# Performance work log

Hardware: AMD Instinct MI355X
Metric: run time of the kernel (lower is better)

Reference implementation:

```python
import jax, jax.numpy as jnp
import numpy as np

N_NODES = 100000


def gcn_conv(x, W, b, src, dst, n):
    """PyG GCNConv: add self-loops, symmetric degree norm, linear, scatter-add."""
    loop = jnp.arange(n, dtype=src.dtype)
    s = jnp.concatenate([src, loop])  # source nodes (message origin)
    d = jnp.concatenate([dst, loop])  # target nodes (aggregation)
    deg = jax.ops.segment_sum(jnp.ones_like(d, dtype=x.dtype), d, num_segments=n)
    dinv = jnp.where(deg > 0, jax.lax.rsqrt(deg), 0.0)
    norm = dinv[s] * dinv[d]  # [E+N]
    h = x @ W  # [N, out]
    msg = h[s] * norm[:, None]  # [E+N, out]
    return jax.ops.segment_sum(msg, d, num_segments=n) + b


def setup_inputs() -> dict:
    key = jax.random.key(0)
    ks = jax.random.split(key, 8)
    n, e, din, dh, dout = N_NODES, 3200000, 128, 64, 6
    x = jax.random.normal(ks[0], (n, din), dtype=jnp.float32)
    edge_index = jax.random.randint(ks[1], (2, e), 0, n, dtype=jnp.int64)
    sc = lambda f: 1.0 / np.sqrt(f)
    W1 = jax.random.normal(ks[2], (din, dh), dtype=jnp.float32) * sc(din)
    b1 = jnp.zeros((dh,), dtype=jnp.float32)
    W2 = jax.random.normal(ks[3], (dh, dh), dtype=jnp.float32) * sc(dh)
    b2 = jnp.zeros((dh,), dtype=jnp.float32)
    W3 = jax.random.normal(ks[4], (dh, dout), dtype=jnp.float32) * sc(dh)
    b3 = jnp.zeros((dout,), dtype=jnp.float32)
    return {"x": x, "edge_index": edge_index, "W1": W1, "b1": b1,
            "W2": W2, "b2": b2, "W3": W3, "b3": b3}


def reference(x, edge_index, W1, b1, W2, b2, W3, b3):
    n = x.shape[0]
    src, dst = edge_index[0], edge_index[1]
    # eval mode: dropout is identity
    h = jax.nn.relu(gcn_conv(x, W1, b1, src, dst, n))
    h = jax.nn.relu(gcn_conv(h, W2, b2, src, dst, n))
    h = gcn_conv(h, W3, b3, src, dst, n)
    return jax.nn.log_softmax(h, axis=1)
```

## Files before the change

### kernel.cpp

```cpp
#include <hip/hip_runtime.h>
#include <hip/hip_fp16.h>
#include <math.h>


#define WS_ALIGN(x) (((x) + 255) & ~(size_t)255)
#define BKN 128
#define CAP 4608
#define EPT 8
#define BIN_THR 512
#define BIN_CHUNK (BIN_THR * EPT)

typedef _Float16 half8 __attribute__((ext_vector_type(8)));
typedef float floatx4 __attribute__((ext_vector_type(4)));

__global__ __launch_bounds__(BIN_THR) void bin_kernel(
    const int* __restrict__ src, const int* __restrict__ dst,
    int* __restrict__ cur, int* __restrict__ slab, int E, int NB) {
    __shared__ int counts[784];
    const int tid = threadIdx.x;
    const int base = blockIdx.x * BIN_CHUNK + tid * EPT;
    for (int i = tid; i < NB; i += BIN_THR) counts[i] = 0;
    __syncthreads();
    int b[EPT], w[EPT], lpos[EPT];
    #pragma unroll
    for (int k = 0; k < EPT; ++k) {
        int e = base + k;
        if (e < E) {
            int s = src[e], d = dst[e];
            b[k] = d >> 7;
            w[k] = (s << 7) | (d & 127);
        } else b[k] = -1;
    }
    #pragma unroll
    for (int k = 0; k < EPT; ++k)
        if (b[k] >= 0) lpos[k] = atomicAdd(&counts[b[k]], 1);
    __syncthreads();
    for (int i = tid; i < NB; i += BIN_THR) {
        int c = counts[i];
        counts[i] = c ? atomicAdd(&cur[i], c) : 0;
    }
    __syncthreads();
    #pragma unroll
    for (int k = 0; k < EPT; ++k) {
        if (b[k] >= 0) {
            int pos = counts[b[k]] + lpos[k];
            if (pos < CAP) slab[(size_t)b[k] * CAP + pos] = w[k];
        }
    }
}

__global__ __launch_bounds__(512) void bucket_sort_kernel(
    const int* __restrict__ slab, const int* __restrict__ cur,
    int* __restrict__ srcS, int2* __restrict__ rows,
    float* __restrict__ dinv, int n) {
    __shared__ int cnt[BKN], s[BKN], cursor[BKN];
    const int b = blockIdx.x, tid = threadIdx.x;
    const int m = min(cur[b], CAP);
    const int* sp = slab + (size_t)b * CAP;
    if (tid < BKN) cnt[tid] = 0;
    __syncthreads();
    for (int j = tid; j < m; j += 512) atomicAdd(&cnt[sp[j] & (BKN - 1)], 1);
    __syncthreads();
    if (tid < BKN) s[tid] = cnt[tid];
    __syncthreads();
    for (int off = 1; off < BKN; off <<= 1) {
        int v = 0;
        if (tid < BKN && tid >= off) v = s[tid - off];
        __syncthreads();
        if (tid < BKN) s[tid] += v;
        __syncthreads();
    }
    if (tid < BKN) {
        int ofs = s[tid] - cnt[tid];
        cursor[tid] = ofs;
        int node = b * BKN + tid;
        if (node < n) {
            rows[node] = make_int2(b * CAP + ofs, b * CAP + ofs + cnt[tid]);
            dinv[node] = rsqrtf((float)(cnt[tid] + 1));
        }
    }
    __syncthreads();
    for (int j = tid; j < m; j += 512) {
        int w = sp[j];
        int p = atomicAdd(&cursor[w & (BKN - 1)], 1);
        srcS[(size_t)b * CAP + p] = w >> 7;
    }
}

template <int K>
__global__ __launch_bounds__(256) void linear_mfma_f32_kernel(
    const float* __restrict__ Xf, const float* __restrict__ W,
    const float* __restrict__ dinv, _Float16* __restrict__ Y, int n) {
    constexpr int KC = K / 32;
    __shared__ _Float16 Bf[KC * 4 * 64 * 8];
    const int tid = threadIdx.x;
    for (int i = tid; i < KC * 4 * 64 * 8; i += 256) {
        int j = i & 7, lane = (i >> 3) & 63, tile = (i >> 9) & 3, kc = i >> 11;
        int k = kc * 32 + ((lane >> 4) << 3) + j;
        int col = tile * 16 + (lane & 15);
        Bf[i] = (_Float16)W[k * 64 + col];
    }
    __syncthreads();
    const int lane = tid & 63, wid = tid >> 6;
    const int mrow = lane & 15, quad = lane >> 4;
    #pragma unroll
    for (int tt = 0; tt < 4; ++tt) {
        const int base = (blockIdx.x * 4 + tt) * 64 + wid * 16;
        if (base >= n) continue;
        const int anode = min(base + mrow, n - 1);
        floatx4 acc[4] = {{0, 0, 0, 0}, {0, 0, 0, 0}, {0, 0, 0, 0}, {0, 0, 0, 0}};
        #pragma unroll
        for (int kc = 0; kc < KC; ++kc) {
            float4 xa = *(const float4*)&Xf[(size_t)anode * K + kc * 32 + quad * 8];
            float4 xb = *(const float4*)&Xf[(size_t)anode * K + kc * 32 + quad * 8 + 4];
            half8 a;
            a[0] = (_Float16)xa.x; a[1] = (_Float16)xa.y; a[2] = (_Float16)xa.z; a[3] = (_Float16)xa.w;
            a[4] = (_Float16)xb.x; a[5] = (_Float16)xb.y; a[6] = (_Float16)xb.z; a[7] = (_Float16)xb.w;
            #pragma unroll
            for (int t = 0; t < 4; ++t) {
                half8 b = *(const half8*)&Bf[((kc * 4 + t) * 64 + lane) * 8];
                acc[t] = __builtin_amdgcn_mfma_f32_16x16x32_f16(a, b, acc[t], 0, 0, 0);
            }
        }
        #pragma unroll
        for (int r = 0; r < 4; ++r) {
            int node = base + quad * 4 + r;
            if (node < n) {
                float di = dinv[node];
                #pragma unroll
                for (int t = 0; t < 4; ++t)
                    Y[(size_t)node * 64 + t * 16 + mrow] = (_Float16)(acc[t][r] * di);
            }
        }
    }
}

__global__ __launch_bounds__(256) void linear_mfma_f16_kernel(
    const _Float16* __restrict__ Xh, const float* __restrict__ W,
    const float* __restrict__ dinv, _Float16* __restrict__ Y, int n) {
    constexpr int K = 64, KC = 2;
    __shared__ _Float16 Bf[KC * 4 * 64 * 8];
    const int tid = threadIdx.x;
    for (int i = tid; i < KC * 4 * 64 * 8; i += 256) {
        int j = i & 7, lane = (i >> 3) & 63, tile = (i >> 9) & 3, kc = i >> 11;
        int k = kc * 32 + ((lane >> 4) << 3) + j;
        int col = tile * 16 + (lane & 15);
        Bf[i] = (_Float16)W[k * 64 + col];
    }
    __syncthreads();
    const int lane = tid & 63, wid = tid >> 6;
    const int mrow = lane & 15, quad = lane >> 4;
    #pragma unroll
    for (int tt = 0; tt < 4; ++tt) {
        const int base = (blockIdx.x * 4 + tt) * 64 + wid * 16;
        if (base >= n) continue;
        const int anode = min(base + mrow, n - 1);
        floatx4 acc[4] = {{0, 0, 0, 0}, {0, 0, 0, 0}, {0, 0, 0, 0}, {0, 0, 0, 0}};
        #pragma unroll
        for (int kc = 0; kc < KC; ++kc) {
            half8 a = *(const half8*)&Xh[(size_t)anode * K + kc * 32 + quad * 8];
            #pragma unroll
            for (int t = 0; t < 4; ++t) {
                half8 b = *(const half8*)&Bf[((kc * 4 + t) * 64 + lane) * 8];
                acc[t] = __builtin_amdgcn_mfma_f32_16x16x32_f16(a, b, acc[t], 0, 0, 0);
            }
        }
        #pragma unroll
        for (int r = 0; r < 4; ++r) {
            int node = base + quad * 4 + r;
            if (node < n) {
                float di = dinv[node];
                #pragma unroll
                for (int t = 0; t < 4; ++t)
                    Y[(size_t)node * 64 + t * 16 + mrow] = (_Float16)(acc[t][r] * di);
            }
        }
    }
}

__global__ __launch_bounds__(256) void linear3_kernel(const __half* __restrict__ Xh,
                                                      const float* __restrict__ W,
                                                      const float* __restrict__ dinv,
                                                      __half* __restrict__ Y, int n) {
    __shared__ float Wl[64 * 6];
    __shared__ float Xs[32][65];
    const int tid = threadIdx.x;
    for (int i = tid; i < 64 * 6; i += 256) Wl[i] = W[i];
    const int sub = tid >> 3;
    const int feat = tid & 7;
    for (int base = blockIdx.x * 32; base < n; base += gridDim.x * 32) {
        __syncthreads();
        for (int i = tid; i < 32 * 64; i += 256) {
            int r = i >> 6, c = i & 63;
            int node = base + r;
            Xs[r][c] = (node < n) ? __half2float(Xh[(size_t)node * 64 + c]) : 0.f;
        }
        __syncthreads();
        int node = base + sub;
        if (node < n) {
            float r = 0.f;
            if (feat < 6) {
                float acc = 0.f;
                #pragma unroll
                for (int k = 0; k < 64; ++k) acc = fmaf(Xs[sub][k], Wl[k * 6 + feat], acc);
                r = acc * dinv[node];
            }
            Y[(size_t)node * 8 + feat] = __float2half_rn(r);
        }
    }
}

__global__ __launch_bounds__(256) void agg64_kernel(
    const _Float16* __restrict__ Hs, const float* __restrict__ dinv,
    const int* __restrict__ srcS, const int2* __restrict__ rows,
    const float* __restrict__ bias, _Float16* __restrict__ Out,
    int n, int do_relu) {
    const int wave = (blockIdx.x * blockDim.x + threadIdx.x) >> 6;
    const int lane = threadIdx.x & 63;
    if (wave >= n) return;
    const int slot = lane >> 3;
    const int f8 = lane & 7;
    const int2 row = rows[wave];
    const int beg = row.x, end = row.y;
    half8 hA, hB;
    #pragma unroll
    for (int i = 0; i < 8; ++i) { hA[i] = (_Float16)0.f; hB[i] = (_Float16)0.f; }
    int j = beg;
    for (; j + 32 <= end; j += 32) {
        int s0 = srcS[j      + slot];
        int s1 = srcS[j + 8  + slot];
        int s2 = srcS[j + 16 + slot];
        int s3 = srcS[j + 24 + slot];
        half8 v0 = *(const half8*)&Hs[(size_t)s0 * 64 + f8 * 8];
        half8 v1 = *(const half8*)&Hs[(size_t)s1 * 64 + f8 * 8];
        half8 v2 = *(const half8*)&Hs[(size_t)s2 * 64 + f8 * 8];
        half8 v3 = *(const half8*)&Hs[(size_t)s3 * 64 + f8 * 8];
        hA += v0; hB += v1; hA += v2; hB += v3;
    }
    for (; j + 16 <= end; j += 16) {
        int s0 = srcS[j + slot];
        int s1 = srcS[j + 8 + slot];
        half8 v0 = *(const half8*)&Hs[(size_t)s0 * 64 + f8 * 8];
        half8 v1 = *(const half8*)&Hs[(size_t)s1 * 64 + f8 * 8];
        hA += v0; hB += v1;
    }
    for (; j < end; j += 8) {
        int jj = j + slot;
        if (jj < end) {
            half8 v = *(const half8*)&Hs[(size_t)srcS[jj] * 64 + f8 * 8];
            hA += v;
        }
    }
    half8 ht = hA + hB;
    #pragma unroll
    for (int mask = 8; mask <= 32; mask <<= 1) {
        int4 ci = *(int4*)&ht, oi;
        oi.x = __shfl_xor(ci.x, mask);
        oi.y = __shfl_xor(ci.y, mask);
        oi.z = __shfl_xor(ci.z, mask);
        oi.w = __shfl_xor(ci.w, mask);
        ht += *(half8*)&oi;
    }
    half8 self = *(const half8*)&Hs[(size_t)wave * 64 + f8 * 8];
    const float di = dinv[wave];
    float4 b0 = *(const float4*)&bias[f8 * 8];
    float4 b1 = *(const float4*)&bias[f8 * 8 + 4];
    float bb[8] = {b0.x, b0.y, b0.z, b0.w, b1.x, b1.y, b1.z, b1.w};
    half8 o;
    #pragma unroll
    for (int i = 0; i < 8; ++i) {
        float t = ((float)ht[i] + (float)self[i]) * di + bb[i];
        if (do_relu) t = fmaxf(t, 0.f);
        o[i] = (_Float16)t;
    }
    if (slot == 0) *(half8*)&Out[(size_t)wave * 64 + f8 * 8] = o;
}

__global__ __launch_bounds__(256) void agg6_lsm_kernel(
    const _Float16* __restrict__ Hs6, const float* __restrict__ dinv,
    const int* __restrict__ srcS, const int2* __restrict__ rows,
    const float* __restrict__ bias, float* __restrict__ out, int n) {
    const int wave = (blockIdx.x * blockDim.x + threadIdx.x) >> 6;
    const int lane = threadIdx.x & 63;
    if (wave >= n) return;
    const int2 row = rows[wave];
    const int beg = row.x, end = row.y;
    half8 ht;
    #pragma unroll
    for (int i = 0; i < 8; ++i) ht[i] = (_Float16)0.f;
    for (int j = beg + lane; j < end; j += 64) {
        int s = srcS[j];
        ht += *(const half8*)&Hs6[(size_t)s * 8];
    }
    #pragma unroll
    for (int mask = 1; mask <= 32; mask <<= 1) {
        int4 ci = *(int4*)&ht, oi;
        oi.x = __shfl_xor(ci.x, mask);
        oi.y = __shfl_xor(ci.y, mask);
        oi.z = __shfl_xor(ci.z, mask);
        oi.w = __shfl_xor(ci.w, mask);
        ht += *(half8*)&oi;
    }
    half8 self = *(const half8*)&Hs6[(size_t)wave * 8];
    const float di = dinv[wave];
    float a[6];
    #pragma unroll
    for (int q = 0; q < 6; ++q)
        a[q] = ((float)ht[q] + (float)self[q]) * di + bias[q];
    float mx = a[0];
    #pragma unroll
    for (int q = 1; q < 6; ++q) mx = fmaxf(mx, a[q]);
    float sum = 0.f;
    #pragma unroll
    for (int q = 0; q < 6; ++q) sum += expf(a[q] - mx);
    float lse = mx + logf(sum);
    if (lane == 0) {
        float* op = &out[(size_t)wave * 6];
        *(float2*)(op)     = make_float2(a[0] - lse, a[1] - lse);
        *(float2*)(op + 2) = make_float2(a[2] - lse, a[3] - lse);
        *(float2*)(op + 4) = make_float2(a[4] - lse, a[5] - lse);
    }
}

extern "C" void kernel_launch(void* const* d_in, const int* in_sizes, int n_in,
                              void* d_out, int out_size, void* d_ws, size_t ws_size,
                              hipStream_t stream) {
    const float* x  = (const float*)d_in[0];
    const int*   ei = (const int*)d_in[1];
    const float* W1 = (const float*)d_in[2];
    const float* b1 = (const float*)d_in[3];
    const float* W2 = (const float*)d_in[4];
    const float* b2 = (const float*)d_in[5];
    const float* W3 = (const float*)d_in[6];
    const float* b3 = (const float*)d_in[7];
    float* out = (float*)d_out;

    const int n = in_sizes[0] / 128;
    const int E = in_sizes[1] / 2;
    const int* src = ei;
    const int* dst = ei + E;
    const int NB = (n + BKN - 1) / BKN;

    char* ws = (char*)d_ws;
    auto carve = [&](size_t bytes) { char* p = ws; ws += WS_ALIGN(bytes); return p; };
    int*      cur  = (int*)     carve((size_t)NB * 4);
    float*    dinv = (float*)   carve((size_t)n * 4);
    int*      slab = (int*)     carve((size_t)NB * CAP * 4);
    int*      srcS = (int*)     carve((size_t)NB * CAP * 4);
    int2*     rows = (int2*)    carve((size_t)n * 8);
    _Float16* hsA  = (_Float16*)carve((size_t)n * 64 * 2 + 4096);
    _Float16* hsB  = (_Float16*)carve((size_t)n * 64 * 2 + 4096);
    _Float16* hsC  = (_Float16*)carve((size_t)n * 8 * 2);
    (void)ws_size; (void)n_in; (void)out_size;

    hipMemsetAsync(cur, 0, (size_t)NB * 4, stream);
    bin_kernel<<<(E + BIN_CHUNK - 1) / BIN_CHUNK, BIN_THR, 0, stream>>>(src, dst, cur, slab, E, NB);
    bucket_sort_kernel<<<NB, 512, 0, stream>>>(slab, cur, srcS, rows, dinv, n);

    const int aggGrid = (n + 3) / 4;
    const int linGrid = (n + 255) / 256;

    linear_mfma_f32_kernel<128><<<linGrid, 256, 0, stream>>>(x, W1, dinv, hsA, n);
    agg64_kernel<<<aggGrid, 256, 0, stream>>>(hsA, dinv, srcS, rows, b1, hsB, n, 1);

    linear_mfma_f16_kernel<<<linGrid, 256, 0, stream>>>(hsB, W2, dinv, hsA, n);
    agg64_kernel<<<aggGrid, 256, 0, stream>>>(hsA, dinv, srcS, rows, b2, hsB, n, 1);

    linear3_kernel<<<2048, 256, 0, stream>>>((const __half*)hsB, W3, dinv, (__half*)hsC, n);
    agg6_lsm_kernel<<<aggGrid, 256, 0, stream>>>(hsC, dinv, srcS, rows, b3, out, n);
}
```

Baseline: 357.5 us.

## Aggregate eight nodes per wave with degree-sorted node order for balance

Result: no change. 364.3 us (+1.9%).

```diff
diff --git a/kernel.cpp b/kernel.cpp
--- a/kernel.cpp
+++ b/kernel.cpp
@@ -52,7 +52,7 @@
 __global__ __launch_bounds__(512) void bucket_sort_kernel(
     const int* __restrict__ slab, const int* __restrict__ cur,
     int* __restrict__ srcS, int2* __restrict__ rows,
-    float* __restrict__ dinv, int n) {
+    float* __restrict__ dinv, int* __restrict__ nodeOrd, int n) {
     __shared__ int cnt[BKN], s[BKN], cursor[BKN];
     const int b = blockIdx.x, tid = threadIdx.x;
     const int m = min(cur[b], CAP);
@@ -71,13 +71,20 @@
         __syncthreads();
     }
     if (tid < BKN) {
-        int ofs = s[tid] - cnt[tid];
+        int c = cnt[tid];
+        int ofs = s[tid] - c;
         cursor[tid] = ofs;
         int node = b * BKN + tid;
         if (node < n) {
-            rows[node] = make_int2(b * CAP + ofs, b * CAP + ofs + cnt[tid]);
-            dinv[node] = rsqrtf((float)(cnt[tid] + 1));
-        }
+            rows[node] = make_int2(b * CAP + ofs, b * CAP + ofs + c);
+            dinv[node] = rsqrtf((float)(c + 1));
+        }
+        int rank = 0;
+        for (int u = 0; u < BKN; ++u) {
+            int cu = cnt[u];
+            rank += (cu > c) || (cu == c && u < tid);
+        }
+        if (node < n) nodeOrd[b * BKN + rank] = node;
     }
     __syncthreads();
     for (int j = tid; j < m; j += 512) {
@@ -213,47 +220,73 @@
 __global__ __launch_bounds__(256) void agg64_kernel(
     const _Float16* __restrict__ Hs, const float* __restrict__ dinv,
     const int* __restrict__ srcS, const int2* __restrict__ rows,
-    const float* __restrict__ bias, _Float16* __restrict__ Out,
-    int n, int do_relu) {
-    const int wave = (blockIdx.x * blockDim.x + threadIdx.x) >> 6;
+    const int* __restrict__ nodeOrd, const float* __restrict__ bias,
+    _Float16* __restrict__ Out, int n, int do_relu) {
+    const int widx = (blockIdx.x * blockDim.x + threadIdx.x) >> 6;
     const int lane = threadIdx.x & 63;
-    if (wave >= n) return;
-    const int slot = lane >> 3;
+    const int g = lane >> 3;
     const int f8 = lane & 7;
-    const int2 row = rows[wave];
-    const int beg = row.x, end = row.y;
-    half8 hA, hB;
-    #pragma unroll
-    for (int i = 0; i < 8; ++i) { hA[i] = (_Float16)0.f; hB[i] = (_Float16)0.f; }
-    int j = beg;
-    for (; j + 32 <= end; j += 32) {
-        int s0 = srcS[j      + slot];
-        int s1 = srcS[j + 8  + slot];
-        int s2 = srcS[j + 16 + slot];
-        int s3 = srcS[j + 24 + slot];
-        half8 v0 = *(const half8*)&Hs[(size_t)s0 * 64 + f8 * 8];
-        half8 v1 = *(const half8*)&Hs[(size_t)s1 * 64 + f8 * 8];
-        half8 v2 = *(const half8*)&Hs[(size_t)s2 * 64 + f8 * 8];
-        half8 v3 = *(const half8*)&Hs[(size_t)s3 * 64 + f8 * 8];
-        hA += v0; hB += v1; hA += v2; hB += v3;
-    }
-    for (; j + 16 <= end; j += 16) {
-        int s0 = srcS[j + slot];
-        int s1 = srcS[j + 8 + slot];
-        half8 v0 = *(const half8*)&Hs[(size_t)s0 * 64 + f8 * 8];
-        half8 v1 = *(const half8*)&Hs[(size_t)s1 * 64 + f8 * 8];
-        hA += v0; hB += v1;
-    }
-    for (; j < end; j += 8) {
-        int jj = j + slot;
-        if (jj < end) {
-            half8 v = *(const half8*)&Hs[(size_t)srcS[jj] * 64 + f8 * 8];
-            hA += v;
-        }
-    }
-    half8 ht = hA + hB;
-    #pragma unroll
-    for (int mask = 8; mask <= 32; mask <<= 1) {
+    const int idx = widx * 8 + g;
+    int node = 0;
+    int2 row = make_int2(0, 0);
+    if (idx < n) { node = nodeOrd[idx]; row = rows[node]; }
+    const char* HsB = (const char*)Hs;
+    const unsigned fo = (unsigned)(f8 << 4);
+    half8 h0, h1;
+    #pragma unroll
+    for (int i = 0; i < 8; ++i) { h0[i] = (_Float16)0.f; h1[i] = (_Float16)0.f; }
+    int jb = row.x;
+    const int je = row.y;
+    for (; jb + 4 <= je; jb += 4) {
+        int s0 = srcS[jb], s1 = srcS[jb + 1], s2 = srcS[jb + 2], s3 = srcS[jb + 3];
+        half8 v0 = *(const half8*)(HsB + (((unsigned)s0) << 7) + fo);
+        half8 v1 = *(const half8*)(HsB + (((unsigned)s1) << 7) + fo);
+        half8 v2 = *(const half8*)(HsB + (((unsigned)s2) << 7) + fo);
+        half8 v3 = *(const half8*)(HsB + (((unsigned)s3) << 7) + fo);
+        h0 += v0; h1 += v1; h0 += v2; h1 += v3;
+    }
+    for (; jb < je; ++jb) {
+        half8 v = *(const half8*)(HsB + (((unsigned)srcS[jb]) << 7) + fo);
+        h0 += v;
+    }
+    half8 ht = h0 + h1;
+    half8 self = *(const half8*)(HsB + (((unsigned)node) << 7) + fo);
+    const float di = (idx < n) ? dinv[node] : 0.f;
+    float4 b0 = *(const float4*)&bias[f8 * 8];
+    float4 b1 = *(const float4*)&bias[f8 * 8 + 4];
+    float bb[8] = {b0.x, b0.y, b0.z, b0.w, b1.x, b1.y, b1.z, b1.w};
+    half8 o;
+    #pragma unroll
+    for (int i = 0; i < 8; ++i) {
+        float t = ((float)ht[i] + (float)self[i]) * di + bb[i];
+        if (do_relu) t = fmaxf(t, 0.f);
+        o[i] = (_Float16)t;
+    }
+    if (idx < n)
+        *(half8*)((char*)Out + (((unsigned)node) << 7) + fo) = o;
+}
+
+__global__ __launch_bounds__(256) void agg6_lsm_kernel(
+    const _Float16* __restrict__ Hs6, const float* __restrict__ dinv,
+    const int* __restrict__ srcS, const int2* __restrict__ rows,
+    const int* __restrict__ nodeOrd, const float* __restrict__ bias,
+    float* __restrict__ out, int n) {
+    const int widx = (blockIdx.x * blockDim.x + threadIdx.x) >> 6;
+    const int lane = threadIdx.x & 63;
+    const int g = lane >> 3;
+    const int l = lane & 7;
+    const int idx = widx * 8 + g;
+    int node = 0;
+    int2 row = make_int2(0, 0);
+    if (idx < n) { node = nodeOrd[idx]; row = rows[node]; }
+    const char* HsB = (const char*)Hs6;
+    half8 ht;
+    #pragma unroll
+    for (int i = 0; i < 8; ++i) ht[i] = (_Float16)0.f;
+    for (int j = row.x + l; j < row.y; j += 8)
+        ht += *(const half8*)(HsB + (((unsigned)srcS[j]) << 4));
+    #pragma unroll
+    for (int mask = 1; mask <= 4; mask <<= 1) {
         int4 ci = *(int4*)&ht, oi;
         oi.x = __shfl_xor(ci.x, mask);
         oi.y = __shfl_xor(ci.y, mask);
@@ -261,48 +294,8 @@
         oi.w = __shfl_xor(ci.w, mask);
         ht += *(half8*)&oi;
     }
-    half8 self = *(const half8*)&Hs[(size_t)wave * 64 + f8 * 8];
-    const float di = dinv[wave];
-    float4 b0 = *(const float4*)&bias[f8 * 8];
-    float4 b1 = *(const float4*)&bias[f8 * 8 + 4];
-    float bb[8] = {b0.x, b0.y, b0.z, b0.w, b1.x, b1.y, b1.z, b1.w};
-    half8 o;
-    #pragma unroll
-    for (int i = 0; i < 8; ++i) {
-        float t = ((float)ht[i] + (float)self[i]) * di + bb[i];
-        if (do_relu) t = fmaxf(t, 0.f);
-        o[i] = (_Float16)t;
-    }
-    if (slot == 0) *(half8*)&Out[(size_t)wave * 64 + f8 * 8] = o;
-}
-
-__global__ __launch_bounds__(256) void agg6_lsm_kernel(
-    const _Float16* __restrict__ Hs6, const float* __restrict__ dinv,
-    const int* __restrict__ srcS, const int2* __restrict__ rows,
-    const float* __restrict__ bias, float* __restrict__ out, int n) {
-    const int wave = (blockIdx.x * blockDim.x + threadIdx.x) >> 6;
-    const int lane = threadIdx.x & 63;
-    if (wave >= n) return;
-    const int2 row = rows[wave];
-    const int beg = row.x, end = row.y;
-    half8 ht;
-    #pragma unroll
-    for (int i = 0; i < 8; ++i) ht[i] = (_Float16)0.f;
-    for (int j = beg + lane; j < end; j += 64) {
-        int s = srcS[j];
-        ht += *(const half8*)&Hs6[(size_t)s * 8];
-    }
-    #pragma unroll
-    for (int mask = 1; mask <= 32; mask <<= 1) {
-        int4 ci = *(int4*)&ht, oi;
-        oi.x = __shfl_xor(ci.x, mask);
-        oi.y = __shfl_xor(ci.y, mask);
-        oi.z = __shfl_xor(ci.z, mask);
-        oi.w = __shfl_xor(ci.w, mask);
-        ht += *(half8*)&oi;
-    }
-    half8 self = *(const half8*)&Hs6[(size_t)wave * 8];
-    const float di = dinv[wave];
+    half8 self = *(const half8*)(HsB + (((unsigned)node) << 4));
+    const float di = (idx < n) ? dinv[node] : 0.f;
     float a[6];
     #pragma unroll
     for (int q = 0; q < 6; ++q)
@@ -314,8 +307,8 @@
     #pragma unroll
     for (int q = 0; q < 6; ++q) sum += expf(a[q] - mx);
     float lse = mx + logf(sum);
-    if (lane == 0) {
-        float* op = &out[(size_t)wave * 6];
+    if (l == 0 && idx < n) {
+        float* op = &out[(size_t)node * 6];
         *(float2*)(op)     = make_float2(a[0] - lse, a[1] - lse);
         *(float2*)(op + 2) = make_float2(a[2] - lse, a[3] - lse);
         *(float2*)(op + 4) = make_float2(a[4] - lse, a[5] - lse);
@@ -343,29 +336,30 @@
 
     char* ws = (char*)d_ws;
     auto carve = [&](size_t bytes) { char* p = ws; ws += WS_ALIGN(bytes); return p; };
-    int*      cur  = (int*)     carve((size_t)NB * 4);
-    float*    dinv = (float*)   carve((size_t)n * 4);
-    int*      slab = (int*)     carve((size_t)NB * CAP * 4);
-    int*      srcS = (int*)     carve((size_t)NB * CAP * 4);
-    int2*     rows = (int2*)    carve((size_t)n * 8);
-    _Float16* hsA  = (_Float16*)carve((size_t)n * 64 * 2 + 4096);
-    _Float16* hsB  = (_Float16*)carve((size_t)n * 64 * 2 + 4096);
-    _Float16* hsC  = (_Float16*)carve((size_t)n * 8 * 2);
+    int*      cur     = (int*)     carve((size_t)NB * 4);
+    float*    dinv    = (float*)   carve((size_t)n * 4);
+    int*      slab    = (int*)     carve((size_t)NB * CAP * 4);
+    int*      srcS    = (int*)     carve((size_t)NB * CAP * 4);
+    int2*     rows    = (int2*)    carve((size_t)n * 8);
+    int*      nodeOrd = (int*)     carve((size_t)NB * BKN * 4);
+    _Float16* hsA     = (_Float16*)carve((size_t)n * 64 * 2 + 4096);
+    _Float16* hsB     = (_Float16*)carve((size_t)n * 64 * 2 + 4096);
+    _Float16* hsC     = (_Float16*)carve((size_t)n * 8 * 2);
     (void)ws_size; (void)n_in; (void)out_size;
 
     hipMemsetAsync(cur, 0, (size_t)NB * 4, stream);
     bin_kernel<<<(E + BIN_CHUNK - 1) / BIN_CHUNK, BIN_THR, 0, stream>>>(src, dst, cur, slab, E, NB);
-    bucket_sort_kernel<<<NB, 512, 0, stream>>>(slab, cur, srcS, rows, dinv, n);
-
-    const int aggGrid = (n + 3) / 4;
+    bucket_sort_kernel<<<NB, 512, 0, stream>>>(slab, cur, srcS, rows, dinv, nodeOrd, n);
+
+    const int aggGrid = (n + 31) / 32;
     const int linGrid = (n + 255) / 256;
 
     linear_mfma_f32_kernel<128><<<linGrid, 256, 0, stream>>>(x, W1, dinv, hsA, n);
-    agg64_kernel<<<aggGrid, 256, 0, stream>>>(hsA, dinv, srcS, rows, b1, hsB, n, 1);
+    agg64_kernel<<<aggGrid, 256, 0, stream>>>(hsA, dinv, srcS, rows, nodeOrd, b1, hsB, n, 1);
 
     linear_mfma_f16_kernel<<<linGrid, 256, 0, stream>>>(hsB, W2, dinv, hsA, n);
-    agg64_kernel<<<aggGrid, 256, 0, stream>>>(hsA, dinv, srcS, rows, b2, hsB, n, 1);
+    agg64_kernel<<<aggGrid, 256, 0, stream>>>(hsA, dinv, srcS, rows, nodeOrd, b2, hsB, n, 1);
 
     linear3_kernel<<<2048, 256, 0, stream>>>((const __half*)hsB, W3, dinv, (__half*)hsC, n);
-    agg6_lsm_kernel<<<aggGrid, 256, 0, stream>>>(hsC, dinv, srcS, rows, b3, out, n);
-}
+    agg6_lsm_kernel<<<aggGrid, 256, 0, stream>>>(hsC, dinv, srcS, rows, nodeOrd, b3, out, n);
+}
```
